# Kernel tuning notes

Hardware: AMD Instinct MI355X
Metric: run time of the kernel (lower is better)

The kernel has to match this reference:

```python
import jax, jax.numpy as jnp
import numpy as np

VOCAB = 50000
D = 512          # in_feat == word_embedding_dim
B = 4096
S = 128
NUM_LABELS = 3


def setup_inputs() -> dict:
    key = jax.random.key(0)
    ks = jax.random.split(key, 16)
    ids_a = jax.random.randint(ks[0], (B, S), 0, VOCAB, dtype=jnp.int32)
    ids_b = jax.random.randint(ks[1], (B, S), 0, VOCAB, dtype=jnp.int32)
    mask_a = jax.random.randint(ks[2], (B, S), 0, 2) > 0
    mask_b = jax.random.randint(ks[3], (B, S), 0, 2) > 0
    s = 0.02
    W_emb = jax.random.normal(ks[4], (VOCAB, D), jnp.float32) * s
    W_emb = W_emb.at[0].set(0.0)  # padding_idx=0
    enc_w1 = jax.random.normal(ks[5], (D, D), jnp.float32) * s
    enc_b1 = jnp.zeros((D,), jnp.float32)
    enc_w2 = jax.random.normal(ks[6], (D, D), jnp.float32) * s
    enc_b2 = jnp.zeros((D,), jnp.float32)
    cls_w1 = jax.random.normal(ks[7], (2 * D, D), jnp.float32) * s
    cls_b1 = jnp.zeros((D,), jnp.float32)
    cls_w2 = jax.random.normal(ks[8], (D, NUM_LABELS), jnp.float32) * s
    cls_b2 = jnp.zeros((NUM_LABELS,), jnp.float32)
    return {
        "text_a_inputs_id": ids_a, "text_b_inputs_id": ids_b,
        "text_a_attention_mask": mask_a, "text_b_attention_mask": mask_b,
        "W_emb": W_emb,
        "enc_w1": enc_w1, "enc_b1": enc_b1, "enc_w2": enc_w2, "enc_b2": enc_b2,
        "cls_w1": cls_w1, "cls_b1": cls_b1, "cls_w2": cls_w2, "cls_b2": cls_b2,
    }


def _encode(ids, mask, W_emb, w1, b1, w2, b2):
    # embedding gather [B,S,D], fused masked sum-pool -> [B,D]
    emb = W_emb[ids]
    pooled = jnp.einsum("bsd,bs->bd", emb, mask.astype(emb.dtype))
    x = jnp.tanh(pooled @ w1 + b1)
    x = jnp.tanh(x @ w2 + b2)  # dropout is identity in eval
    return x


def reference(text_a_inputs_id, text_b_inputs_id, text_a_attention_mask,
              text_b_attention_mask, W_emb, enc_w1, enc_b1, enc_w2, enc_b2,
              cls_w1, cls_b1, cls_w2, cls_b2):
    va = _encode(text_a_inputs_id, text_a_attention_mask, W_emb, enc_w1, enc_b1, enc_w2, enc_b2)
    vb = _encode(text_b_inputs_id, text_b_attention_mask, W_emb, enc_w1, enc_b1, enc_w2, enc_b2)
    pooled = jnp.concatenate([va, vb], axis=-1)  # [B, 2D]
    h = jnp.tanh(pooled @ cls_w1 + cls_b1)
    logits = h @ cls_w2 + cls_b2  # [B, num_labels]
    return logits
```

## Files before the change

### kernel.cpp

```cpp
#include <hip/hip_runtime.h>


typedef unsigned short u16;
typedef __attribute__((ext_vector_type(8))) short short8;
typedef __attribute__((ext_vector_type(4))) float f32x4;

__device__ __forceinline__ float bfu2f(u16 u) {
    union { unsigned int i; float f; } v;
    v.i = ((unsigned int)u) << 16;
    return v.f;
}

__device__ __forceinline__ u16 f2bfu(float f) {
    union { float f; unsigned int i; } v;
    v.f = f;
    unsigned int x = v.i;
    x += 0x7fffu + ((x >> 16) & 1u);
    return (u16)(x >> 16);
}

__device__ __forceinline__ float fast_tanh(float x) {
    float xc = fminf(fmaxf(x, -15.f), 15.f);
    float e = __builtin_amdgcn_exp2f(xc * 2.885390082f);
    return (e - 1.f) / (e + 1.f);
}

__device__ __forceinline__ int detect_wave(const u16* __restrict__ W,
                                           const unsigned int* __restrict__ m,
                                           int lane)
{
    int cnt = 0;
    int w01 = 1, b01 = 1, lo16 = 0;
    #pragma unroll
    for (int j = lane; j < 256; j += 64) {
        u16 u = W[1024 + 2 * j];
        int e = (u >> 7) & 0xFF;
        cnt += (e >= 0x6A && e <= 0x7E) ? 1 : 0;
        unsigned int v = m[j];
        w01 &= (v <= 1u) ? 1 : 0;
        b01 &= ((v & ~0x01010101u) == 0u) ? 1 : 0;
        lo16 |= ((v & 0xFFFFu) == 0x3F80u) ? 1 : 0;
    }
    #pragma unroll
    for (int off = 32; off > 0; off >>= 1) {
        cnt  += __shfl_down(cnt, off);
        w01  &= __shfl_down(w01, off);
        b01  &= __shfl_down(b01, off);
        lo16 |= __shfl_down(lo16, off);
    }
    int mtype;
    if (w01)        mtype = 0;
    else if (b01)   mtype = 1;
    else if (lo16)  mtype = 2;
    else            mtype = 3;
    int fl = ((cnt >= 128) ? 1 : 0) | (mtype << 2);
    return __shfl(fl, 0);
}

__device__ __forceinline__ int mask_nonzero(const void* __restrict__ msk,
                                            int idx, int mtype)
{
    switch (mtype) {
        case 0:  return ((const int*)msk)[idx] != 0;
        case 1:  return ((const unsigned char*)msk)[idx] != 0;
        case 2:  return ((const u16*)msk)[idx] != 0;
        default: return ((const unsigned int*)msk)[idx] != 0u;
    }
}

__global__ __launch_bounds__(128) void pool_kernel(
    const int* __restrict__ ids_a, const int* __restrict__ ids_b,
    const void* __restrict__ mska, const void* __restrict__ mskb,
    const void* __restrict__ W, u16* __restrict__ P,
    float* __restrict__ outz,
    const unsigned int* __restrict__ Mdet)
{
    __shared__ int s_ids[128];
    __shared__ int s_cnt;
    __shared__ int s_flags;
    __shared__ float sP[512];
    const int t = threadIdx.x;
    const int w = t >> 6;
    const int lane = t & 63;

    if (blockIdx.x < 96) outz[blockIdx.x * 128 + t] = 0.f;

    if (t == 0) s_cnt = 0;
    if (t < 64) {
        int fl = detect_wave((const u16*)W, Mdet, t);
        if (t == 0) s_flags = fl;
    }
    __syncthreads();
    const int  flags = s_flags;
    const bool isbf  = (flags & 1) != 0;
    const int  mtype = (flags >> 2) & 3;

    const int row = blockIdx.x;
    const int r   = row & 4095;
    const int* __restrict__ ids = (row < 4096) ? ids_a : ids_b;
    const void* __restrict__ msk = (row < 4096) ? mska : mskb;

    int id = ids[r * 128 + t];
    int mk = mask_nonzero(msk, r * 128 + t, mtype);
    if (mk) {
        int idx = atomicAdd(&s_cnt, 1);
        s_ids[idx] = id;
    }
    __syncthreads();
    const int cnt = s_cnt;

    float acc[8] = {};
    if (isbf) {
        const u16* Wb = (const u16*)W;
        int j = w;
        for (; j + 14 < cnt; j += 16) {
            union { uint4 v; u16 s[8]; } r0, r1, r2, r3, r4, r5, r6, r7;
            r0.v = *(const uint4*)(Wb + (size_t)s_ids[j + 0]  * 512 + lane * 8);
            r1.v = *(const uint4*)(Wb + (size_t)s_ids[j + 2]  * 512 + lane * 8);
            r2.v = *(const uint4*)(Wb + (size_t)s_ids[j + 4]  * 512 + lane * 8);
            r3.v = *(const uint4*)(Wb + (size_t)s_ids[j + 6]  * 512 + lane * 8);
            r4.v = *(const uint4*)(Wb + (size_t)s_ids[j + 8]  * 512 + lane * 8);
            r5.v = *(const uint4*)(Wb + (size_t)s_ids[j + 10] * 512 + lane * 8);
            r6.v = *(const uint4*)(Wb + (size_t)s_ids[j + 12] * 512 + lane * 8);
            r7.v = *(const uint4*)(Wb + (size_t)s_ids[j + 14] * 512 + lane * 8);
            #pragma unroll
            for (int i = 0; i < 8; ++i)
                acc[i] += ((bfu2f(r0.s[i]) + bfu2f(r1.s[i])) +
                           (bfu2f(r2.s[i]) + bfu2f(r3.s[i]))) +
                          ((bfu2f(r4.s[i]) + bfu2f(r5.s[i])) +
                           (bfu2f(r6.s[i]) + bfu2f(r7.s[i])));
        }
        for (; j + 6 < cnt; j += 8) {
            union { uint4 v; u16 s[8]; } r0, r1, r2, r3;
            r0.v = *(const uint4*)(Wb + (size_t)s_ids[j + 0] * 512 + lane * 8);
            r1.v = *(const uint4*)(Wb + (size_t)s_ids[j + 2] * 512 + lane * 8);
            r2.v = *(const uint4*)(Wb + (size_t)s_ids[j + 4] * 512 + lane * 8);
            r3.v = *(const uint4*)(Wb + (size_t)s_ids[j + 6] * 512 + lane * 8);
            #pragma unroll
            for (int i = 0; i < 8; ++i)
                acc[i] += bfu2f(r0.s[i]) + bfu2f(r1.s[i]) +
                          bfu2f(r2.s[i]) + bfu2f(r3.s[i]);
        }
        for (; j < cnt; j += 2) {
            union { uint4 v; u16 s[8]; } rr;
            rr.v = *(const uint4*)(Wb + (size_t)s_ids[j] * 512 + lane * 8);
            #pragma unroll
            for (int i = 0; i < 8; ++i) acc[i] += bfu2f(rr.s[i]);
        }
    } else {
        const float* Wf = (const float*)W;
        for (int j = w; j < cnt; j += 2) {
            const float* rp = Wf + (size_t)s_ids[j] * 512 + lane * 8;
            float4 a = *(const float4*)(rp + 0);
            float4 b = *(const float4*)(rp + 4);
            acc[0] += a.x; acc[1] += a.y; acc[2] += a.z; acc[3] += a.w;
            acc[4] += b.x; acc[5] += b.y; acc[6] += b.z; acc[7] += b.w;
        }
    }

    if (w == 0) {
        #pragma unroll
        for (int i = 0; i < 8; ++i) sP[lane * 8 + i] = acc[i];
    }
    __syncthreads();
    if (w == 1) {
        union { uint4 v; u16 s[8]; } o;
        #pragma unroll
        for (int i = 0; i < 8; ++i)
            o.s[i] = f2bfu(acc[i] + sP[lane * 8 + i]);
        *(uint4*)(P + (size_t)row * 512 + lane * 8) = o.v;
    }
}

#define GEMM_KLOOP_BK64                                                        \
    FETCH(0)                                                                   \
    STORE(0)                                                                   \
    FETCH(64)                                                                  \
    __syncthreads();                                                           \
    int p = 0;                                                                 \
    for (int k0 = 0; k0 < K; k0 += 64) {                                       \
        if (k0 + 64 < K) {                                                     \
            STORE(p ^ 1)                                                       \
            if (k0 + 128 < K) FETCH(k0 + 128)                                  \
        }                                                                      \
        const u16* Ap  = As0 + p * 9216;                                       \
        const u16* Bp2 = Bs0 + p * 4608;                                       \
        short8 af0[2], af1[2], bf0[2], bf1[2];                                 \
        _Pragma("unroll")                                                      \
        for (int i = 0; i < 2; ++i) {                                          \
            af0[i] = *(const short8*)&Ap[(wm + i * 16 + lm) * 72 + kq * 8];    \
            af1[i] = *(const short8*)&Ap[(wm + i * 16 + lm) * 72 + 32 + kq * 8];\
        }                                                                      \
        _Pragma("unroll")                                                      \
        for (int j = 0; j < 2; ++j) {                                          \
            const int n = wn + j * 16 + lm;                                    \
            bf0[j] = *(const short8*)&Bp2[n * 72 + ((kq + (n >> 3)) & 7) * 8]; \
            bf1[j] = *(const short8*)&Bp2[n * 72 + ((4 + kq + (n >> 3)) & 7) * 8];\
        }                                                                      \
        _Pragma("unroll")                                                      \
        for (int i = 0; i < 2; ++i)                                            \
            _Pragma("unroll")                                                  \
            for (int j = 0; j < 2; ++j) {                                      \
                acc[i][j] = __builtin_amdgcn_mfma_f32_16x16x32_bf16(           \
                    af0[i], bf0[j], acc[i][j], 0, 0, 0);                       \
                acc[i][j] = __builtin_amdgcn_mfma_f32_16x16x32_bf16(           \
                    af1[i], bf1[j], acc[i][j], 0, 0, 0);                       \
            }                                                                  \
        if (k0 + 64 < K) __syncthreads();                                      \
        p ^= 1;                                                                \
    }

#define GEMM_FETCH_STORE_BK64                                                  \
    uint4 ra0, ra1, rbb;                                                       \
    float4 rf0, rf1;                                                           \
    (void)rf0; (void)rf1;

#define FETCH(k0)                                                             \
    {                                                                         \
        const int kg = (k0) + ac;                                             \
        const u16* base = (kg < K1) ? (A + kg) : (A2 + (kg - K1));            \
        ra0 = *(const uint4*)(base + (size_t)(m0 + ar) * 512);                \
        ra1 = *(const uint4*)(base + (size_t)(m0 + ar + 64) * 512);           \
        if constexpr (ISBF) {                                                 \
            rbb = *(const uint4*)(Bb + (size_t)((k0) + bkr) * 512 + n0 + nb); \
        } else {                                                              \
            const float* Bp_ = Bf + (size_t)((k0) + bkr) * 512 + n0 + nb;     \
            rf0 = *(const float4*)(Bp_ + 0);                                  \
            rf1 = *(const float4*)(Bp_ + 4);                                  \
        }                                                                     \
    }

#define STORE(pp)                                                             \
    {                                                                         \
        *(uint4*)&As0[(pp) * 9216 + ar * 72 + ac] = ra0;                      \
        *(uint4*)&As0[(pp) * 9216 + (ar + 64) * 72 + ac] = ra1;               \
        u16 bvals[8];                                                         \
        if constexpr (ISBF) {                                                 \
            union { uint4 v; u16 s[8]; } ub; ub.v = rbb;                      \
            _Pragma("unroll")                                                 \
            for (int i = 0; i < 8; ++i) bvals[i] = ub.s[i];                   \
        } else {                                                              \
            bvals[0] = f2bfu(rf0.x); bvals[1] = f2bfu(rf0.y);                 \
            bvals[2] = f2bfu(rf0.z); bvals[3] = f2bfu(rf0.w);                 \
            bvals[4] = f2bfu(rf1.x); bvals[5] = f2bfu(rf1.y);                 \
            bvals[6] = f2bfu(rf1.z); bvals[7] = f2bfu(rf1.w);                 \
        }                                                                     \
        const int slot_ = (((bkr >> 3) + jn) & 7) * 8 + (bkr & 7);            \
        _Pragma("unroll")                                                     \
        for (int i = 0; i < 8; ++i)                                           \
            Bs0[(pp) * 4608 + (nb + i) * 72 + slot_] = bvals[i];              \
    }

template<bool ISBF>
__device__ __forceinline__ void gemm_tile(
    const u16* __restrict__ A, const u16* __restrict__ A2, const int K1,
    const void* __restrict__ Bv, const void* __restrict__ biasv,
    u16* __restrict__ C, const int K, const int m0, const int n0,
    u16* __restrict__ As0, u16* __restrict__ Bs0)
{
    const int tid  = threadIdx.x;
    const int lane = tid & 63;
    const int wid = tid >> 6;
    const int wm  = (wid & 3) * 32;
    const int wn  = (wid >> 2) * 32;
    const int ar  = tid >> 3;
    const int ac  = (tid & 7) * 8;
    const int bkr = tid >> 3;
    const int jn  = tid & 7;
    const int nb  = jn * 8;
    const int lm = lane & 15;
    const int kq = lane >> 4;

    const u16*   Bb = (const u16*)Bv;
    const float* Bf = (const float*)Bv;

    f32x4 acc[2][2];
    #pragma unroll
    for (int i = 0; i < 2; ++i)
        #pragma unroll
        for (int j = 0; j < 2; ++j)
            acc[i][j] = (f32x4){0.f, 0.f, 0.f, 0.f};

    GEMM_FETCH_STORE_BK64
    GEMM_KLOOP_BK64

    #pragma unroll
    for (int j = 0; j < 2; ++j) {
        const int n = n0 + wn + j * 16 + lm;
        const float bsv = ISBF ? bfu2f(((const u16*)biasv)[n])
                               : ((const float*)biasv)[n];
        #pragma unroll
        for (int i = 0; i < 2; ++i) {
            #pragma unroll
            for (int r = 0; r < 4; ++r) {
                const int m = m0 + wm + i * 16 + kq * 4 + r;
                C[(size_t)m * 512 + n] = f2bfu(fast_tanh(acc[i][j][r] + bsv));
            }
        }
    }
}

__global__ __launch_bounds__(512, 4) void gemm_mfma(
    const u16* __restrict__ A, const u16* __restrict__ A2, int K1,
    const void* __restrict__ B, const void* __restrict__ bias,
    u16* __restrict__ C, int K,
    const u16* __restrict__ Wdet, const unsigned int* __restrict__ Mdet)
{
    __shared__ __align__(16) u16 As[2 * 128 * 72];
    __shared__ __align__(16) u16 Bs[2 * 64 * 72];
    __shared__ int s_flags;

    if (threadIdx.x < 64) {
        int fl = detect_wave(Wdet, Mdet, threadIdx.x);
        if (threadIdx.x == 0) s_flags = fl;
    }
    __syncthreads();
    const int m0 = blockIdx.x * 128;
    const int n0 = blockIdx.y * 64;
    if (s_flags & 1) gemm_tile<true >(A, A2, K1, B, bias, C, K, m0, n0, As, Bs);
    else             gemm_tile<false>(A, A2, K1, B, bias, C, K, m0, n0, As, Bs);
}

template<bool ISBF>
__device__ __forceinline__ void g3_body(
    const u16* __restrict__ A, const u16* __restrict__ A2, const int K1,
    const void* __restrict__ Bv, const void* __restrict__ biasv,
    const void* __restrict__ w2v, const void* __restrict__ cb2v,
    float* __restrict__ outp, const int K,
    u16* __restrict__ As0, u16* __restrict__ Bs0)
{
    const int tid  = threadIdx.x;
    const int lane = tid & 63;
    const int wid = tid >> 6;
    const int wm  = (wid & 3) * 32;
    const int wn  = (wid >> 2) * 32;
    const int ar  = tid >> 3;
    const int ac  = (tid & 7) * 8;
    const int bkr = tid >> 3;
    const int jn  = tid & 7;
    const int nb  = jn * 8;
    const int lm = lane & 15;
    const int kq = lane >> 4;
    const int m0 = (blockIdx.x & 31) * 128;
    const int n0 = (blockIdx.x >> 5) * 64;

    const u16*   Bb = (const u16*)Bv;
    const float* Bf = (const float*)Bv;

    f32x4 acc[2][2];
    #pragma unroll
    for (int i = 0; i < 2; ++i)
        #pragma unroll
        for (int j = 0; j < 2; ++j)
            acc[i][j] = (f32x4){0.f, 0.f, 0.f, 0.f};

    GEMM_FETCH_STORE_BK64
    GEMM_KLOOP_BK64

    float lg[2][4][3];
    #pragma unroll
    for (int i = 0; i < 2; ++i)
        #pragma unroll
        for (int r = 0; r < 4; ++r)
            #pragma unroll
            for (int l = 0; l < 3; ++l) lg[i][r][l] = 0.f;

    #pragma unroll
    for (int j = 0; j < 2; ++j) {
        const int n = n0 + wn + j * 16 + lm;
        const float bsv = ISBF ? bfu2f(((const u16*)biasv)[n])
                               : ((const float*)biasv)[n];
        float wc[3];
        #pragma unroll
        for (int l = 0; l < 3; ++l)
            wc[l] = ISBF ? bfu2f(((const u16*)w2v)[n * 3 + l])
                         : ((const float*)w2v)[n * 3 + l];
        #pragma unroll
        for (int i = 0; i < 2; ++i)
            #pragma unroll
            for (int r = 0; r < 4; ++r) {
                const float h = fast_tanh(acc[i][j][r] + bsv);
                #pragma unroll
                for (int l = 0; l < 3; ++l) lg[i][r][l] += h * wc[l];
            }
    }
    #pragma unroll
    for (int off = 1; off <= 8; off <<= 1)
        #pragma unroll
        for (int i = 0; i < 2; ++i)
            #pragma unroll
            for (int r = 0; r < 4; ++r)
                #pragma unroll
                for (int l = 0; l < 3; ++l)
                    lg[i][r][l] += __shfl_xor(lg[i][r][l], off);

    if (lm == 0) {
        const bool addb = (n0 == 0) && (wn == 0);
        float cb[3];
        #pragma unroll
        for (int l = 0; l < 3; ++l)
            cb[l] = ISBF ? bfu2f(((const u16*)cb2v)[l])
                         : ((const float*)cb2v)[l];
        #pragma unroll
        for (int i = 0; i < 2; ++i)
            #pragma unroll
            for (int r = 0; r < 4; ++r) {
                const int m = m0 + wm + i * 16 + kq * 4 + r;
                #pragma unroll
                for (int l = 0; l < 3; ++l) {
                    float v = lg[i][r][l];
                    if (addb) v += cb[l];
                    atomicAdd(&outp[m * 3 + l], v);
                }
            }
    }
}

__global__ __launch_bounds__(512, 4) void gemm3_logits(
    const u16* __restrict__ A, const u16* __restrict__ A2, int K1,
    const void* __restrict__ B, const void* __restrict__ bias,
    const void* __restrict__ w2, const void* __restrict__ cb2,
    float* __restrict__ out, int K,
    const u16* __restrict__ Wdet, const unsigned int* __restrict__ Mdet)
{
    __shared__ __align__(16) u16 As[2 * 128 * 72];
    __shared__ __align__(16) u16 Bs[2 * 64 * 72];
    __shared__ int s_flags;

    if (threadIdx.x < 64) {
        int fl = detect_wave(Wdet, Mdet, threadIdx.x);
        if (threadIdx.x == 0) s_flags = fl;
    }
    __syncthreads();
    if (s_flags & 1)
        g3_body<true >(A, A2, K1, B, bias, w2, cb2, out, K, As, Bs);
    else
        g3_body<false>(A, A2, K1, B, bias, w2, cb2, out, K, As, Bs);
}

extern "C" void kernel_launch(void* const* d_in, const int* in_sizes, int n_in,
                              void* d_out, int out_size, void* d_ws, size_t ws_size,
                              hipStream_t stream)
{
    const int* ids_a  = (const int*)d_in[0];
    const int* ids_b  = (const int*)d_in[1];
    const void* mask_a = d_in[2];
    const void* mask_b = d_in[3];
    const void* W_emb  = d_in[4];
    const void* enc_w1 = d_in[5];
    const void* enc_b1 = d_in[6];
    const void* enc_w2 = d_in[7];
    const void* enc_b2 = d_in[8];
    const void* cls_w1 = d_in[9];
    const void* cls_b1 = d_in[10];
    const void* cls_w2 = d_in[11];
    const void* cls_b2 = d_in[12];

    const u16* Wdet = (const u16*)W_emb;
    const unsigned int* Mdet = (const unsigned int*)mask_a;

    u16* buf0 = (u16*)d_ws;
    u16* buf1 = buf0 + (size_t)8192 * 512;
    float* outp = (float*)d_out;

    pool_kernel<<<8192, 128, 0, stream>>>(ids_a, ids_b, mask_a, mask_b,
                                          W_emb, buf0, outp, Mdet);

    gemm_mfma<<<dim3(64, 8), 512, 0, stream>>>(
        buf0, buf0, 512, enc_w1, enc_b1, buf1, 512, Wdet, Mdet);

    gemm_mfma<<<dim3(64, 8), 512, 0, stream>>>(
        buf1, buf1, 512, enc_w2, enc_b2, buf0, 512, Wdet, Mdet);

    gemm3_logits<<<256, 512, 0, stream>>>(
        buf0, buf0 + (size_t)4096 * 512, 512, cls_w1, cls_b1,
        cls_w2, cls_b2, outp, 1024, Wdet, Mdet);
}
```

Before: 354.1 us.

## Split embedding pooling across column slices with one wave per slice

Launches eight 64-thread blocks per row, each owning a 64-column slice of the embedding, instead of one 128-thread block splitting tokens across two waves. This removes the shared-memory cross-wave reduction and one barrier, and raises block count for latency hiding. In exchange, each lane issues scalar 2-byte gathers instead of 16-byte vector loads. The id/mask compaction and format detection are repeated in every slice block.

```diff
diff --git a/kernel.cpp b/kernel.cpp
--- a/kernel.cpp
+++ b/kernel.cpp
@@ -68,108 +68,79 @@
     }
 }
 
-__global__ __launch_bounds__(128) void pool_kernel(
+__global__ __launch_bounds__(64) void pool_kernel(
     const int* __restrict__ ids_a, const int* __restrict__ ids_b,
     const void* __restrict__ mska, const void* __restrict__ mskb,
     const void* __restrict__ W, u16* __restrict__ P,
     float* __restrict__ outz,
     const unsigned int* __restrict__ Mdet)
 {
-    __shared__ int s_ids[128];
+    __shared__ int s_ids[132];
     __shared__ int s_cnt;
-    __shared__ int s_flags;
-    __shared__ float sP[512];
-    const int t = threadIdx.x;
-    const int w = t >> 6;
-    const int lane = t & 63;
-
-    if (blockIdx.x < 96) outz[blockIdx.x * 128 + t] = 0.f;
+    const int t     = threadIdx.x;
+    const int bid   = blockIdx.x;
+    const int slice = bid & 7;
+    const int row   = bid >> 3;
+    const int r     = row & 4095;
+
+    if (slice == 7 && row < 96) {
+        outz[row * 128 + t]      = 0.f;
+        outz[row * 128 + 64 + t] = 0.f;
+    }
 
     if (t == 0) s_cnt = 0;
-    if (t < 64) {
-        int fl = detect_wave((const u16*)W, Mdet, t);
-        if (t == 0) s_flags = fl;
-    }
-    __syncthreads();
-    const int  flags = s_flags;
-    const bool isbf  = (flags & 1) != 0;
-    const int  mtype = (flags >> 2) & 3;
-
-    const int row = blockIdx.x;
-    const int r   = row & 4095;
+    const int fl = detect_wave((const u16*)W, Mdet, t);
+    const bool isbf  = (fl & 1) != 0;
+    const int  mtype = (fl >> 2) & 3;
+
     const int* __restrict__ ids = (row < 4096) ? ids_a : ids_b;
     const void* __restrict__ msk = (row < 4096) ? mska : mskb;
 
-    int id = ids[r * 128 + t];
-    int mk = mask_nonzero(msk, r * 128 + t, mtype);
-    if (mk) {
-        int idx = atomicAdd(&s_cnt, 1);
-        s_ids[idx] = id;
+    __syncthreads();
+    {
+        const int id0 = ids[r * 128 + t];
+        const int id1 = ids[r * 128 + 64 + t];
+        if (mask_nonzero(msk, r * 128 + t, mtype))
+            s_ids[atomicAdd(&s_cnt, 1)] = id0;
+        if (mask_nonzero(msk, r * 128 + 64 + t, mtype))
+            s_ids[atomicAdd(&s_cnt, 1)] = id1;
     }
     __syncthreads();
     const int cnt = s_cnt;
 
-    float acc[8] = {};
+    const int col = slice * 64 + t;
+    float acc = 0.f;
     if (isbf) {
-        const u16* Wb = (const u16*)W;
-        int j = w;
-        for (; j + 14 < cnt; j += 16) {
-            union { uint4 v; u16 s[8]; } r0, r1, r2, r3, r4, r5, r6, r7;
-            r0.v = *(const uint4*)(Wb + (size_t)s_ids[j + 0]  * 512 + lane * 8);
-            r1.v = *(const uint4*)(Wb + (size_t)s_ids[j + 2]  * 512 + lane * 8);
-            r2.v = *(const uint4*)(Wb + (size_t)s_ids[j + 4]  * 512 + lane * 8);
-            r3.v = *(const uint4*)(Wb + (size_t)s_ids[j + 6]  * 512 + lane * 8);
-            r4.v = *(const uint4*)(Wb + (size_t)s_ids[j + 8]  * 512 + lane * 8);
-            r5.v = *(const uint4*)(Wb + (size_t)s_ids[j + 10] * 512 + lane * 8);
-            r6.v = *(const uint4*)(Wb + (size_t)s_ids[j + 12] * 512 + lane * 8);
-            r7.v = *(const uint4*)(Wb + (size_t)s_ids[j + 14] * 512 + lane * 8);
-            #pragma unroll
-            for (int i = 0; i < 8; ++i)
-                acc[i] += ((bfu2f(r0.s[i]) + bfu2f(r1.s[i])) +
-                           (bfu2f(r2.s[i]) + bfu2f(r3.s[i]))) +
-                          ((bfu2f(r4.s[i]) + bfu2f(r5.s[i])) +
-                           (bfu2f(r6.s[i]) + bfu2f(r7.s[i])));
+        const u16* __restrict__ Wb = (const u16*)W + col;
+        int j = 0;
+        for (; j + 7 < cnt; j += 8) {
+            const u16 v0 = Wb[(size_t)s_ids[j + 0] * 512];
+            const u16 v1 = Wb[(size_t)s_ids[j + 1] * 512];
+            const u16 v2 = Wb[(size_t)s_ids[j + 2] * 512];
+            const u16 v3 = Wb[(size_t)s_ids[j + 3] * 512];
+            const u16 v4 = Wb[(size_t)s_ids[j + 4] * 512];
+            const u16 v5 = Wb[(size_t)s_ids[j + 5] * 512];
+            const u16 v6 = Wb[(size_t)s_ids[j + 6] * 512];
+            const u16 v7 = Wb[(size_t)s_ids[j + 7] * 512];
+            acc += ((bfu2f(v0) + bfu2f(v1)) + (bfu2f(v2) + bfu2f(v3))) +
+                   ((bfu2f(v4) + bfu2f(v5)) + (bfu2f(v6) + bfu2f(v7)));
         }
-        for (; j + 6 < cnt; j += 8) {
-            union { uint4 v; u16 s[8]; } r0, r1, r2, r3;
-            r0.v = *(const uint4*)(Wb + (size_t)s_ids[j + 0] * 512 + lane * 8);
-            r1.v = *(const uint4*)(Wb + (size_t)s_ids[j + 2] * 512 + lane * 8);
-            r2.v = *(const uint4*)(Wb + (size_t)s_ids[j + 4] * 512 + lane * 8);
-            r3.v = *(const uint4*)(Wb + (size_t)s_ids[j + 6] * 512 + lane * 8);
-            #pragma unroll
-            for (int i = 0; i < 8; ++i)
-                acc[i] += bfu2f(r0.s[i]) + bfu2f(r1.s[i]) +
-                          bfu2f(r2.s[i]) + bfu2f(r3.s[i]);
+        for (; j < cnt; ++j)
+            acc += bfu2f(Wb[(size_t)s_ids[j] * 512]);
+    } else {
+        const float* __restrict__ Wf = (const float*)W + col;
+        int j = 0;
+        for (; j + 3 < cnt; j += 4) {
+            const float v0 = Wf[(size_t)s_ids[j + 0] * 512];
+            const float v1 = Wf[(size_t)s_ids[j + 1] * 512];
+            const float v2 = Wf[(size_t)s_ids[j + 2] * 512];
+            const float v3 = Wf[(size_t)s_ids[j + 3] * 512];
+            acc += (v0 + v1) + (v2 + v3);
         }
-        for (; j < cnt; j += 2) {
-            union { uint4 v; u16 s[8]; } rr;
-            rr.v = *(const uint4*)(Wb + (size_t)s_ids[j] * 512 + lane * 8);
-            #pragma unroll
-            for (int i = 0; i < 8; ++i) acc[i] += bfu2f(rr.s[i]);
-        }
-    } else {
-        const float* Wf = (const float*)W;
-        for (int j = w; j < cnt; j += 2) {
-            const float* rp = Wf + (size_t)s_ids[j] * 512 + lane * 8;
-            float4 a = *(const float4*)(rp + 0);
-            float4 b = *(const float4*)(rp + 4);
-            acc[0] += a.x; acc[1] += a.y; acc[2] += a.z; acc[3] += a.w;
-            acc[4] += b.x; acc[5] += b.y; acc[6] += b.z; acc[7] += b.w;
-        }
-    }
-
-    if (w == 0) {
-        #pragma unroll
-        for (int i = 0; i < 8; ++i) sP[lane * 8 + i] = acc[i];
-    }
-    __syncthreads();
-    if (w == 1) {
-        union { uint4 v; u16 s[8]; } o;
-        #pragma unroll
-        for (int i = 0; i < 8; ++i)
-            o.s[i] = f2bfu(acc[i] + sP[lane * 8 + i]);
-        *(uint4*)(P + (size_t)row * 512 + lane * 8) = o.v;
-    }
+        for (; j < cnt; ++j)
+            acc += Wf[(size_t)s_ids[j] * 512];
+    }
+    P[(size_t)row * 512 + col] = f2bfu(acc);
 }
 
 #define GEMM_KLOOP_BK64                                                        \
@@ -463,7 +434,7 @@
     u16* buf1 = buf0 + (size_t)8192 * 512;
     float* outp = (float*)d_out;
 
-    pool_kernel<<<8192, 128, 0, stream>>>(ids_a, ids_b, mask_a, mask_b,
+    pool_kernel<<<65536, 64, 0, stream>>>(ids_a, ids_b, mask_a, mask_b,
                                           W_emb, buf0, outp, Mdet);
 
     gemm_mfma<<<dim3(64, 8), 512, 0, stream>>>(
```

Measured after the change: 333.6 us. 5.8% less time.
